# Optimization experiments

Measured on AMD Instinct MI355X. Metric: run time of the kernel, lower is better.

Reference implementation:

```python
import jax, jax.numpy as jnp
import numpy as np

D_MODEL = 1024
D_HIDDEN = 4096
NUM_EXPERTS = 8
TOP_K = 2


def setup_inputs() -> dict:
    key = jax.random.key(0)
    ks = jax.random.split(key, 7)
    scale_in = 1.0 / np.sqrt(D_MODEL)
    scale_hid = 1.0 / np.sqrt(D_HIDDEN)
    x = jax.random.normal(ks[0], (4, 2048, D_MODEL), dtype=jnp.float32)
    Wr = jax.random.uniform(ks[1], (D_MODEL, NUM_EXPERTS), jnp.float32, -scale_in, scale_in)
    br = jax.random.uniform(ks[2], (NUM_EXPERTS,), jnp.float32, -scale_in, scale_in)
    W1 = jax.random.uniform(ks[3], (NUM_EXPERTS, D_MODEL, D_HIDDEN), jnp.float32, -scale_in, scale_in)
    b1 = jax.random.uniform(ks[4], (NUM_EXPERTS, D_HIDDEN), jnp.float32, -scale_in, scale_in)
    W2 = jax.random.uniform(ks[5], (NUM_EXPERTS, D_HIDDEN, D_MODEL), jnp.float32, -scale_hid, scale_hid)
    b2 = jax.random.uniform(ks[6], (NUM_EXPERTS, D_MODEL), jnp.float32, -scale_hid, scale_hid)
    return {"x": x, "Wr": Wr, "br": br, "W1": W1, "b1": b1, "W2": W2, "b2": b2}


def reference(x, Wr, br, W1, b1, W2, b2):
    B, S, D = x.shape
    E = Wr.shape[1]
    flat = x.reshape(-1, D)                      # [T, D]
    T = flat.shape[0]
    logits = flat @ Wr + br                      # [T, E]
    probs = jax.nn.softmax(logits, axis=-1)
    topk_p, topk_i = jax.lax.top_k(probs, TOP_K)  # [T, K]
    topk_p = topk_p / jnp.sum(topk_p, axis=-1, keepdims=True)
    # combine[t, e] = sum_k topk_p[t, k] * (topk_i[t, k] == e)
    combine = jnp.zeros((T, E), flat.dtype).at[jnp.arange(T)[:, None], topk_i].add(topk_p)
    out = jnp.zeros_like(flat)
    for e in range(E):  # fixed small expert loop; each iter is a dense GEMM pair
        h = jax.nn.relu(flat @ W1[e] + b1[e])    # [T, d_hidden]
        y = h @ W2[e] + b2[e]                    # [T, D]
        out = out + y * combine[:, e:e + 1]
    return out.reshape(B, S, D)
```

## Files before the change

kernel.cpp:

```cpp
#include <hip/hip_runtime.h>
#include <stdint.h>

#define D_MODEL  1024
#define D_HIDDEN 4096
#define NE       8
#define T_TOK    8192
#define BM       128
#define BN       128
#define BK       64
#define MAXT     136
#define ROWS_CAP 17408

typedef __attribute__((ext_vector_type(8))) short short8;
typedef __attribute__((ext_vector_type(4))) float f32x4;

__device__ inline uint16_t f2bf(float f) {
  uint32_t u = __float_as_uint(f);
  uint32_t r = (u + 0x7fffu + ((u >> 16) & 1u)) >> 16;
  return (uint16_t)r;
}

#define GLOAD16(gp, lp) __builtin_amdgcn_global_load_lds( \
  (const __attribute__((address_space(1))) uint32_t*)(gp), \
  (__attribute__((address_space(3))) uint32_t*)(lp), 16, 0, 0)

__global__ void transpose_cvt(const float* __restrict__ in, uint16_t* __restrict__ out,
                              int R, int C) {
  __shared__ float tile[32][33];
  size_t eoff = (size_t)blockIdx.z * R * C;
  in += eoff; out += eoff;
  int c0 = blockIdx.x * 32, r0 = blockIdx.y * 32;
  int x = threadIdx.x, y = threadIdx.y;
#pragma unroll
  for (int i = 0; i < 32; i += 8)
    tile[y + i][x] = in[(size_t)(r0 + y + i) * C + c0 + x];
  __syncthreads();
#pragma unroll
  for (int i = 0; i < 32; i += 8)
    out[(size_t)(c0 + y + i) * R + r0 + x] = f2bf(tile[x][y + i]);
}

__global__ void router_kernel(const float* __restrict__ x, const float* __restrict__ Wr,
                              const float* __restrict__ br,
                              int* __restrict__ cnt, int* __restrict__ tok_of,
                              int* __restrict__ k_of, float* __restrict__ tok_w) {
  int t = blockIdx.x * 4 + (threadIdx.x >> 6);
  int l = threadIdx.x & 63;
  const float* xr = x + (size_t)t * D_MODEL;
  float a[8] = {0.f,0.f,0.f,0.f,0.f,0.f,0.f,0.f};
  for (int d = l; d < D_MODEL; d += 64) {
    float xv = xr[d];
    const float4* w4 = (const float4*)(Wr + d * 8);
    float4 wa = w4[0], wb = w4[1];
    a[0] += xv * wa.x; a[1] += xv * wa.y; a[2] += xv * wa.z; a[3] += xv * wa.w;
    a[4] += xv * wb.x; a[5] += xv * wb.y; a[6] += xv * wb.z; a[7] += xv * wb.w;
  }
#pragma unroll
  for (int e = 0; e < 8; ++e) {
    float v = a[e];
#pragma unroll
    for (int off = 32; off > 0; off >>= 1) v += __shfl_xor(v, off);
    a[e] = v + br[e];
  }
  if (l == 0) {
    int i1 = 0; float v1 = a[0];
#pragma unroll
    for (int e = 1; e < 8; ++e) if (a[e] > v1) { v1 = a[e]; i1 = e; }
    int i2 = -1; float v2 = -1e30f;
#pragma unroll
    for (int e = 0; e < 8; ++e) if (e != i1 && a[e] > v2) { v2 = a[e]; i2 = e; }
    float e2 = __expf(v2 - v1);
    float inv = 1.0f / (1.0f + e2);
    int p1 = atomicAdd(cnt + i1, 1);
    tok_of[i1 * T_TOK + p1] = t; k_of[i1 * T_TOK + p1] = 0;
    int p2 = atomicAdd(cnt + i2, 1);
    tok_of[i2 * T_TOK + p2] = t; k_of[i2 * T_TOK + p2] = 1;
    tok_w[t * 2 + 0] = inv; tok_w[t * 2 + 1] = e2 * inv;
  }
}

__global__ void setup_kernel(const int* __restrict__ cnt, int* __restrict__ meta) {
  if (threadIdx.x != 0 || blockIdx.x != 0) return;
  int base = 0, nt = 0;
  meta[1] = 0;
  for (int e = 0; e < NE; ++e) {
    int c = cnt[e];
    int tiles = (c + BM - 1) / BM;
    for (int i = 0; i < tiles; ++i) {
      meta[16 + nt] = e;
      meta[16 + MAXT + nt] = base + i * BM;
      nt++;
    }
    base += tiles * BM;
    meta[2 + e] = base;
  }
  meta[0] = nt;
}

__global__ void gather_kernel(const float* __restrict__ x, const int* __restrict__ cnt,
                              const int* __restrict__ meta, const int* __restrict__ tok_of,
                              const int* __restrict__ k_of,
                              uint16_t* __restrict__ xp, int* __restrict__ tok2row) {
  int r = blockIdx.x * 4 + (threadIdx.x >> 6);
  int l = threadIdx.x & 63;
  int total = meta[9];
  if (r >= total) return;
  int e = 0;
#pragma unroll
  for (int i = 1; i < 8; ++i) if (r >= meta[1 + i]) e = i;
  int p = r - meta[1 + e];
  uint16_t* dst = xp + (size_t)r * D_MODEL + l * 16;
  if (p < cnt[e]) {
    int t = tok_of[e * T_TOK + p];
    if (l == 0) tok2row[t * 2 + k_of[e * T_TOK + p]] = r;
    const float4* src = (const float4*)(x + (size_t)t * D_MODEL + l * 16);
    short8 o0, o1;
    float4 v0 = src[0], v1 = src[1], v2 = src[2], v3 = src[3];
    o0[0] = (short)f2bf(v0.x); o0[1] = (short)f2bf(v0.y);
    o0[2] = (short)f2bf(v0.z); o0[3] = (short)f2bf(v0.w);
    o0[4] = (short)f2bf(v1.x); o0[5] = (short)f2bf(v1.y);
    o0[6] = (short)f2bf(v1.z); o0[7] = (short)f2bf(v1.w);
    o1[0] = (short)f2bf(v2.x); o1[1] = (short)f2bf(v2.y);
    o1[2] = (short)f2bf(v2.z); o1[3] = (short)f2bf(v2.w);
    o1[4] = (short)f2bf(v3.x); o1[5] = (short)f2bf(v3.y);
    o1[6] = (short)f2bf(v3.z); o1[7] = (short)f2bf(v3.w);
    *(short8*)dst = o0;
    *(short8*)(dst + 8) = o1;
  } else {
    short8 z = {0,0,0,0,0,0,0,0};
    *(short8*)dst = z;
    *(short8*)(dst + 8) = z;
  }
}

template<int KD, int ND, bool RELU_BF16>
__global__ void moe_gemm(const uint16_t* __restrict__ A, const uint16_t* __restrict__ Bt,
                         const float* __restrict__ bias,
                         uint16_t* __restrict__ Cb, float* __restrict__ Cf,
                         const int* __restrict__ meta) {
  int nt = meta[0];
  int mt = blockIdx.y;
  if (mt >= nt) return;
  int e = meta[16 + mt];
  int row0 = meta[16 + MAXT + mt];
  int n0 = blockIdx.x * BN;

  __shared__ __align__(16) uint16_t lA[BM * BK];
  __shared__ __align__(16) uint16_t lB[BN * BK];

  int t = threadIdx.x;
  int w = t >> 6, l = t & 63;
  int wr = (w >> 1) * 64, wc = (w & 1) * 64;

  const uint16_t* Ab = A + (size_t)row0 * KD;
  const uint16_t* Bb = Bt + ((size_t)e * ND + n0) * KD;

  f32x4 acc[4][4];
#pragma unroll
  for (int m = 0; m < 4; ++m)
#pragma unroll
    for (int n = 0; n < 4; ++n) acc[m][n] = (f32x4){0.f, 0.f, 0.f, 0.f};

  int trow = t >> 3;
  int tcol = (t & 7) * 8;
  int scol = tcol ^ ((trow & 7) << 3);

  for (int kt = 0; kt < KD / BK; ++kt) {
    int k0 = kt * BK;
    __syncthreads();
#pragma unroll
    for (int i = 0; i < 4; ++i) {
      GLOAD16(Ab + (size_t)(i * 32 + trow) * KD + k0 + scol, lA + (i * 32 + trow) * BK + tcol);
      GLOAD16(Bb + (size_t)(i * 32 + trow) * KD + k0 + scol, lB + (i * 32 + trow) * BK + tcol);
    }
    asm volatile("s_waitcnt vmcnt(0)" ::: "memory");
    __syncthreads();
#pragma unroll
    for (int kk = 0; kk < 2; ++kk) {
      short8 af[4], bf[4];
      int ko = kk * 32 + (l >> 4) * 8;
      int sw = ((l & 7) << 3);
#pragma unroll
      for (int m = 0; m < 4; ++m)
        af[m] = *(const short8*)(lA + (wr + m * 16 + (l & 15)) * BK + (ko ^ sw));
#pragma unroll
      for (int n = 0; n < 4; ++n)
        bf[n] = *(const short8*)(lB + (wc + n * 16 + (l & 15)) * BK + (ko ^ sw));
#pragma unroll
      for (int m = 0; m < 4; ++m)
#pragma unroll
        for (int n = 0; n < 4; ++n)
          acc[m][n] = __builtin_amdgcn_mfma_f32_16x16x32_bf16(af[m], bf[n], acc[m][n], 0, 0, 0);
    }
  }

#pragma unroll
  for (int m = 0; m < 4; ++m) {
    int row_b = row0 + wr + m * 16 + (l >> 4) * 4;
#pragma unroll
    for (int n = 0; n < 4; ++n) {
      int col = n0 + wc + n * 16 + (l & 15);
      float bv = bias[e * ND + col];
#pragma unroll
      for (int r = 0; r < 4; ++r) {
        float v = acc[m][n][r] + bv;
        size_t off = (size_t)(row_b + r) * ND + col;
        if (RELU_BF16) Cb[off] = f2bf(fmaxf(v, 0.f));
        else           Cf[off] = v;
      }
    }
  }
}

__global__ void combine_kernel(const float* __restrict__ y, const int* __restrict__ tok2row,
                               const float* __restrict__ tok_w, float* __restrict__ out) {
  int t = blockIdx.x;
  int i = threadIdx.x;
  int r0 = tok2row[t * 2], r1 = tok2row[t * 2 + 1];
  float w0 = tok_w[t * 2], w1 = tok_w[t * 2 + 1];
  float4 av = ((const float4*)(y + (size_t)r0 * D_MODEL))[i];
  float4 bv = ((const float4*)(y + (size_t)r1 * D_MODEL))[i];
  float4 res;
  res.x = w0 * av.x + w1 * bv.x;
  res.y = w0 * av.y + w1 * bv.y;
  res.z = w0 * av.z + w1 * bv.z;
  res.w = w0 * av.w + w1 * bv.w;
  ((float4*)(out + (size_t)t * D_MODEL))[i] = res;
}

extern "C" void kernel_launch(void* const* d_in, const int* in_sizes, int n_in,
                              void* d_out, int out_size, void* d_ws, size_t ws_size,
                              hipStream_t stream) {
  const float* x  = (const float*)d_in[0];
  const float* Wr = (const float*)d_in[1];
  const float* br = (const float*)d_in[2];
  const float* W1 = (const float*)d_in[3];
  const float* b1 = (const float*)d_in[4];
  const float* W2 = (const float*)d_in[5];
  const float* b2 = (const float*)d_in[6];
  float* out = (float*)d_out;

  char* ws = (char*)d_ws;
  size_t off = 0;
  auto alloc = [&](size_t bytes) -> void* {
    void* p = ws + off;
    off += (bytes + 255) & ~(size_t)255;
    return p;
  };
  uint16_t* W1T   = (uint16_t*)alloc((size_t)NE * D_MODEL * D_HIDDEN * 2);
  uint16_t* W2T   = (uint16_t*)alloc((size_t)NE * D_MODEL * D_HIDDEN * 2);
  uint16_t* xp    = (uint16_t*)alloc((size_t)ROWS_CAP * D_MODEL * 2);
  uint16_t* hp    = (uint16_t*)alloc((size_t)ROWS_CAP * D_HIDDEN * 2);
  float*    y     = (float*)alloc((size_t)ROWS_CAP * D_MODEL * 4);
  int*      cnt   = (int*)alloc(NE * 4);
  int*      tok_of= (int*)alloc((size_t)NE * T_TOK * 4);
  int*      k_of  = (int*)alloc((size_t)NE * T_TOK * 4);
  float*    tok_w = (float*)alloc(T_TOK * 2 * 4);
  int*      t2r   = (int*)alloc(T_TOK * 2 * 4);
  int*      meta  = (int*)alloc((16 + 2 * MAXT) * 4);

  if (ws_size < off) return;

  hipMemsetAsync(cnt, 0, NE * 4, stream);
  transpose_cvt<<<dim3(D_HIDDEN / 32, D_MODEL / 32, NE), dim3(32, 8), 0, stream>>>(
      W1, W1T, D_MODEL, D_HIDDEN);
  transpose_cvt<<<dim3(D_MODEL / 32, D_HIDDEN / 32, NE), dim3(32, 8), 0, stream>>>(
      W2, W2T, D_HIDDEN, D_MODEL);
  router_kernel<<<T_TOK / 4, 256, 0, stream>>>(x, Wr, br, cnt, tok_of, k_of, tok_w);
  setup_kernel<<<1, 64, 0, stream>>>(cnt, meta);
  gather_kernel<<<ROWS_CAP / 4, 256, 0, stream>>>(x, cnt, meta, tok_of, k_of, xp, t2r);
  moe_gemm<D_MODEL, D_HIDDEN, true><<<dim3(D_HIDDEN / BN, MAXT), 256, 0, stream>>>(
      xp, W1T, b1, hp, nullptr, meta);
  moe_gemm<D_HIDDEN, D_MODEL, false><<<dim3(D_MODEL / BN, MAXT), 256, 0, stream>>>(
      hp, W2T, b2, nullptr, y, meta);
  combine_kernel<<<T_TOK, 256, 0, stream>>>(y, t2r, tok_w, out);
}
```

Baseline: 677.8 us.

## Fuse combine into second GEMM epilogue via atomics; vectorize weight transpose

Removes the intermediate fp32 y buffer and the separate combine kernel. The second expert GEMM now scales each row by its routing weight and atomically adds it into the zeroed output through a row-to-token map built in gather. The weight transpose/convert kernel moves to 64x64 tiles with float4 loads and 16-byte bf16 stores, and the setup kernel builds its tile table in parallel. In exchange, fp32 atomics add contention and make the summation order nondeterministic.

New measurement: 683.8 us. No clear change (+0.9%).

```diff
diff --git a/kernel.cpp b/kernel.cpp
--- a/kernel.cpp
+++ b/kernel.cpp
@@ -26,18 +26,28 @@
 
 __global__ void transpose_cvt(const float* __restrict__ in, uint16_t* __restrict__ out,
                               int R, int C) {
-  __shared__ float tile[32][33];
+  __shared__ float tile[64][65];
   size_t eoff = (size_t)blockIdx.z * R * C;
-  in += eoff; out += eoff;
-  int c0 = blockIdx.x * 32, r0 = blockIdx.y * 32;
-  int x = threadIdx.x, y = threadIdx.y;
-#pragma unroll
-  for (int i = 0; i < 32; i += 8)
-    tile[y + i][x] = in[(size_t)(r0 + y + i) * C + c0 + x];
+  int c0 = blockIdx.x * 64, r0 = blockIdx.y * 64;
+  int t = threadIdx.x;
+  int lr = t >> 4, lc4 = (t & 15) * 4;
+#pragma unroll
+  for (int i = 0; i < 4; ++i) {
+    int rr = i * 16 + lr;
+    float4 v = *(const float4*)(in + eoff + (size_t)(r0 + rr) * C + c0 + lc4);
+    tile[rr][lc4] = v.x; tile[rr][lc4 + 1] = v.y;
+    tile[rr][lc4 + 2] = v.z; tile[rr][lc4 + 3] = v.w;
+  }
   __syncthreads();
-#pragma unroll
-  for (int i = 0; i < 32; i += 8)
-    out[(size_t)(c0 + y + i) * R + r0 + x] = f2bf(tile[x][y + i]);
+  int oc = t >> 3, orr = (t & 7) * 8;
+#pragma unroll
+  for (int i = 0; i < 2; ++i) {
+    int cc = i * 32 + oc;
+    short8 o;
+#pragma unroll
+    for (int j = 0; j < 8; ++j) o[j] = (short)f2bf(tile[orr + j][cc]);
+    *(short8*)(out + eoff + (size_t)(c0 + cc) * R + r0 + orr) = o;
+  }
 }
 
 __global__ void router_kernel(const float* __restrict__ x, const float* __restrict__ Wr,
@@ -80,27 +90,33 @@
 }
 
 __global__ void setup_kernel(const int* __restrict__ cnt, int* __restrict__ meta) {
-  if (threadIdx.x != 0 || blockIdx.x != 0) return;
-  int base = 0, nt = 0;
-  meta[1] = 0;
-  for (int e = 0; e < NE; ++e) {
+  int l = threadIdx.x;
+  int tiles[8], base[9], tpre[9];
+  base[0] = 0; tpre[0] = 0;
+#pragma unroll
+  for (int e = 0; e < 8; ++e) {
     int c = cnt[e];
-    int tiles = (c + BM - 1) / BM;
-    for (int i = 0; i < tiles; ++i) {
-      meta[16 + nt] = e;
-      meta[16 + MAXT + nt] = base + i * BM;
-      nt++;
-    }
-    base += tiles * BM;
-    meta[2 + e] = base;
-  }
-  meta[0] = nt;
+    tiles[e] = (c + BM - 1) / BM;
+    base[e + 1] = base[e] + tiles[e] * BM;
+    tpre[e + 1] = tpre[e] + tiles[e];
+  }
+  int nt = tpre[8];
+  if (l == 0) meta[0] = nt;
+  if (l < 9) meta[1 + l] = base[l];
+  for (int i = l; i < nt; i += 64) {
+    int e = 0;
+#pragma unroll
+    for (int k = 1; k < 8; ++k) if (i >= tpre[k]) e = k;
+    meta[16 + i] = e;
+    meta[16 + MAXT + i] = base[e] + (i - tpre[e]) * BM;
+  }
 }
 
 __global__ void gather_kernel(const float* __restrict__ x, const int* __restrict__ cnt,
                               const int* __restrict__ meta, const int* __restrict__ tok_of,
-                              const int* __restrict__ k_of,
-                              uint16_t* __restrict__ xp, int* __restrict__ tok2row) {
+                              const int* __restrict__ k_of, const float* __restrict__ tok_w,
+                              uint16_t* __restrict__ xp,
+                              int* __restrict__ row2tok, float* __restrict__ row2w) {
   int r = blockIdx.x * 4 + (threadIdx.x >> 6);
   int l = threadIdx.x & 63;
   int total = meta[9];
@@ -112,7 +128,10 @@
   uint16_t* dst = xp + (size_t)r * D_MODEL + l * 16;
   if (p < cnt[e]) {
     int t = tok_of[e * T_TOK + p];
-    if (l == 0) tok2row[t * 2 + k_of[e * T_TOK + p]] = r;
+    if (l == 0) {
+      row2tok[r] = t;
+      row2w[r] = tok_w[t * 2 + k_of[e * T_TOK + p]];
+    }
     const float4* src = (const float4*)(x + (size_t)t * D_MODEL + l * 16);
     short8 o0, o1;
     float4 v0 = src[0], v1 = src[1], v2 = src[2], v3 = src[3];
@@ -127,16 +146,18 @@
     *(short8*)dst = o0;
     *(short8*)(dst + 8) = o1;
   } else {
+    if (l == 0) { row2tok[r] = -1; row2w[r] = 0.f; }
     short8 z = {0,0,0,0,0,0,0,0};
     *(short8*)dst = z;
     *(short8*)(dst + 8) = z;
   }
 }
 
-template<int KD, int ND, bool RELU_BF16>
+template<int KD, int ND, bool FUSED_OUT>
 __global__ void moe_gemm(const uint16_t* __restrict__ A, const uint16_t* __restrict__ Bt,
                          const float* __restrict__ bias,
-                         uint16_t* __restrict__ Cb, float* __restrict__ Cf,
+                         uint16_t* __restrict__ Cb, float* __restrict__ out,
+                         const int* __restrict__ row2tok, const float* __restrict__ row2w,
                          const int* __restrict__ meta) {
   int nt = meta[0];
   int mt = blockIdx.y;
@@ -194,38 +215,41 @@
     }
   }
 
-#pragma unroll
-  for (int m = 0; m < 4; ++m) {
-    int row_b = row0 + wr + m * 16 + (l >> 4) * 4;
-#pragma unroll
-    for (int n = 0; n < 4; ++n) {
-      int col = n0 + wc + n * 16 + (l & 15);
-      float bv = bias[e * ND + col];
+  if (!FUSED_OUT) {
+#pragma unroll
+    for (int m = 0; m < 4; ++m) {
+      int row_b = row0 + wr + m * 16 + (l >> 4) * 4;
+#pragma unroll
+      for (int n = 0; n < 4; ++n) {
+        int col = n0 + wc + n * 16 + (l & 15);
+        float bv = bias[e * ND + col];
+#pragma unroll
+        for (int r = 0; r < 4; ++r)
+          Cb[(size_t)(row_b + r) * ND + col] = f2bf(fmaxf(acc[m][n][r] + bv, 0.f));
+      }
+    }
+  } else {
+    float bv[4];
+#pragma unroll
+    for (int n = 0; n < 4; ++n)
+      bv[n] = bias[e * ND + n0 + wc + n * 16 + (l & 15)];
+#pragma unroll
+    for (int m = 0; m < 4; ++m) {
 #pragma unroll
       for (int r = 0; r < 4; ++r) {
-        float v = acc[m][n][r] + bv;
-        size_t off = (size_t)(row_b + r) * ND + col;
-        if (RELU_BF16) Cb[off] = f2bf(fmaxf(v, 0.f));
-        else           Cf[off] = v;
+        int grow = row0 + wr + m * 16 + (l >> 4) * 4 + r;
+        int tok = row2tok[grow];
+        float wgt = row2w[grow];
+        if (tok >= 0) {
+#pragma unroll
+          for (int n = 0; n < 4; ++n) {
+            int col = n0 + wc + n * 16 + (l & 15);
+            atomicAdd(out + (size_t)tok * ND + col, wgt * (acc[m][n][r] + bv[n]));
+          }
+        }
       }
     }
   }
-}
-
-__global__ void combine_kernel(const float* __restrict__ y, const int* __restrict__ tok2row,
-                               const float* __restrict__ tok_w, float* __restrict__ out) {
-  int t = blockIdx.x;
-  int i = threadIdx.x;
-  int r0 = tok2row[t * 2], r1 = tok2row[t * 2 + 1];
-  float w0 = tok_w[t * 2], w1 = tok_w[t * 2 + 1];
-  float4 av = ((const float4*)(y + (size_t)r0 * D_MODEL))[i];
-  float4 bv = ((const float4*)(y + (size_t)r1 * D_MODEL))[i];
-  float4 res;
-  res.x = w0 * av.x + w1 * bv.x;
-  res.y = w0 * av.y + w1 * bv.y;
-  res.z = w0 * av.z + w1 * bv.z;
-  res.w = w0 * av.w + w1 * bv.w;
-  ((float4*)(out + (size_t)t * D_MODEL))[i] = res;
 }
 
 extern "C" void kernel_launch(void* const* d_in, const int* in_sizes, int n_in,
@@ -247,31 +271,32 @@
     off += (bytes + 255) & ~(size_t)255;
     return p;
   };
-  uint16_t* W1T   = (uint16_t*)alloc((size_t)NE * D_MODEL * D_HIDDEN * 2);
-  uint16_t* W2T   = (uint16_t*)alloc((size_t)NE * D_MODEL * D_HIDDEN * 2);
-  uint16_t* xp    = (uint16_t*)alloc((size_t)ROWS_CAP * D_MODEL * 2);
-  uint16_t* hp    = (uint16_t*)alloc((size_t)ROWS_CAP * D_HIDDEN * 2);
-  float*    y     = (float*)alloc((size_t)ROWS_CAP * D_MODEL * 4);
-  int*      cnt   = (int*)alloc(NE * 4);
-  int*      tok_of= (int*)alloc((size_t)NE * T_TOK * 4);
-  int*      k_of  = (int*)alloc((size_t)NE * T_TOK * 4);
-  float*    tok_w = (float*)alloc(T_TOK * 2 * 4);
-  int*      t2r   = (int*)alloc(T_TOK * 2 * 4);
-  int*      meta  = (int*)alloc((16 + 2 * MAXT) * 4);
+  uint16_t* W1T    = (uint16_t*)alloc((size_t)NE * D_MODEL * D_HIDDEN * 2);
+  uint16_t* W2T    = (uint16_t*)alloc((size_t)NE * D_MODEL * D_HIDDEN * 2);
+  uint16_t* xp     = (uint16_t*)alloc((size_t)ROWS_CAP * D_MODEL * 2);
+  uint16_t* hp     = (uint16_t*)alloc((size_t)ROWS_CAP * D_HIDDEN * 2);
+  int*      cnt    = (int*)alloc(NE * 4);
+  int*      tok_of = (int*)alloc((size_t)NE * T_TOK * 4);
+  int*      k_of   = (int*)alloc((size_t)NE * T_TOK * 4);
+  float*    tok_w  = (float*)alloc(T_TOK * 2 * 4);
+  int*      row2tok= (int*)alloc(ROWS_CAP * 4);
+  float*    row2w  = (float*)alloc(ROWS_CAP * 4);
+  int*      meta   = (int*)alloc((16 + 2 * MAXT) * 4);
 
   if (ws_size < off) return;
 
   hipMemsetAsync(cnt, 0, NE * 4, stream);
-  transpose_cvt<<<dim3(D_HIDDEN / 32, D_MODEL / 32, NE), dim3(32, 8), 0, stream>>>(
+  hipMemsetAsync(out, 0, (size_t)out_size * 4, stream);
+  transpose_cvt<<<dim3(D_HIDDEN / 64, D_MODEL / 64, NE), 256, 0, stream>>>(
       W1, W1T, D_MODEL, D_HIDDEN);
-  transpose_cvt<<<dim3(D_MODEL / 32, D_HIDDEN / 32, NE), dim3(32, 8), 0, stream>>>(
+  transpose_cvt<<<dim3(D_MODEL / 64, D_HIDDEN / 64, NE), 256, 0, stream>>>(
       W2, W2T, D_HIDDEN, D_MODEL);
   router_kernel<<<T_TOK / 4, 256, 0, stream>>>(x, Wr, br, cnt, tok_of, k_of, tok_w);
   setup_kernel<<<1, 64, 0, stream>>>(cnt, meta);
-  gather_kernel<<<ROWS_CAP / 4, 256, 0, stream>>>(x, cnt, meta, tok_of, k_of, xp, t2r);
-  moe_gemm<D_MODEL, D_HIDDEN, true><<<dim3(D_HIDDEN / BN, MAXT), 256, 0, stream>>>(
-      xp, W1T, b1, hp, nullptr, meta);
-  moe_gemm<D_HIDDEN, D_MODEL, false><<<dim3(D_MODEL / BN, MAXT), 256, 0, stream>>>(
-      hp, W2T, b2, nullptr, y, meta);
-  combine_kernel<<<T_TOK, 256, 0, stream>>>(y, t2r, tok_w, out);
-}
+  gather_kernel<<<ROWS_CAP / 4, 256, 0, stream>>>(x, cnt, meta, tok_of, k_of, tok_w,
+                                                  xp, row2tok, row2w);
+  moe_gemm<D_MODEL, D_HIDDEN, false><<<dim3(D_HIDDEN / BN, MAXT), 256, 0, stream>>>(
+      xp, W1T, b1, hp, nullptr, nullptr, nullptr, meta);
+  moe_gemm<D_HIDDEN, D_MODEL, true><<<dim3(D_MODEL / BN, MAXT), 256, 0, stream>>>(
+      hp, W2T, b2, nullptr, out, row2tok, row2w, meta);
+}
```
